# Kernel tuning notes

Measured on AMD Instinct MI355X. Metric: run time of the kernel, lower is better.

## Reference

```python
import jax, jax.numpy as jnp
import numpy as np

EMBED_DIM = 1024
NUM_HEADS = 16
HEAD_DIM = EMBED_DIM // NUM_HEADS
FEATURE_EPS = 1e-06
DEN_EPS = 1e-06


def setup_inputs() -> dict:
    key = jax.random.key(0)
    k_x, k_qw, k_qb, k_ow, k_ob = jax.random.split(key, 5)
    b, l = 2, 2048
    x = jax.random.normal(k_x, (b, l, EMBED_DIM), dtype=jnp.float32)
    s = 1.0 / np.sqrt(EMBED_DIM)
    qkv_w = jax.random.uniform(k_qw, (3 * EMBED_DIM, EMBED_DIM), minval=-s, maxval=s, dtype=jnp.float32)
    qkv_b = jax.random.uniform(k_qb, (3 * EMBED_DIM,), minval=-s, maxval=s, dtype=jnp.float32)
    out_w = jax.random.uniform(k_ow, (EMBED_DIM, EMBED_DIM), minval=-s, maxval=s, dtype=jnp.float32)
    out_b = jax.random.uniform(k_ob, (EMBED_DIM,), minval=-s, maxval=s, dtype=jnp.float32)
    return {"x": x, "qkv_w": qkv_w, "qkv_b": qkv_b, "out_w": out_w, "out_b": out_b}


def reference(x, qkv_w, qkv_b, out_w, out_b):
    b, l, e = x.shape
    # qkv projection -> (3, b, h, l, d)
    qkv = (x @ qkv_w.T + qkv_b).reshape(b, l, 3, NUM_HEADS, HEAD_DIM)
    qkv = jnp.transpose(qkv, (2, 0, 3, 1, 4))
    q, k, v = qkv[0], qkv[1], qkv[2]
    # phi(x) = relu(x) + eps
    q = jax.nn.relu(q) + FEATURE_EPS
    k = jax.nn.relu(k) + FEATURE_EPS
    # running outer-product state: (b, h, l, d, d)
    kv = jnp.cumsum(jnp.einsum('bhld,bhle->bhlde', k, v), axis=2)
    k_cum = jnp.cumsum(k, axis=2)
    num = jnp.einsum('bhld,bhlde->bhle', q, kv)
    den = jnp.maximum(jnp.einsum('bhld,bhld->bhl', q, k_cum)[..., None], DEN_EPS)
    out = num / den  # (b, h, l, d)
    out = jnp.transpose(out, (0, 2, 1, 3)).reshape(b, l, e)
    return out @ out_w.T + out_b
```

## Files before the change

### kernel.cpp

```cpp
#include <hip/hip_runtime.h>
#include <hip/hip_bf16.h>
#include <cstdint>

#define B_ 2
#define L_ 2048
#define E_ 1024
#define H_ 16
#define D_ 64
#define N3_ 3072
#define NCHUNK 32
#define CHUNK 64

typedef __attribute__((ext_vector_type(8))) short bf16x8;
typedef __attribute__((ext_vector_type(4))) float f32x4;

__device__ __forceinline__ unsigned short f2bf(float f) {
  unsigned u = __float_as_uint(f);
  unsigned r = (u + 0x7fffu + ((u >> 16) & 1u)) >> 16;
  return (unsigned short)r;
}
__device__ __forceinline__ float bf2f(unsigned short u) {
  return __uint_as_float(((unsigned)u) << 16);
}

__global__ __launch_bounds__(256) void k_cvt_all(
    const float* __restrict__ x, const float* __restrict__ qkv_w,
    const float* __restrict__ out_w, unsigned short* __restrict__ xb,
    unsigned short* __restrict__ wqkv, unsigned short* __restrict__ wout) {
  const int i = blockIdx.x * 256 + threadIdx.x;
  const float* src;
  unsigned short* dst;
  int j;
  if (i < 1048576)      { src = x;     dst = xb;   j = i; }
  else if (i < 1835008) { src = qkv_w; dst = wqkv; j = i - 1048576; }
  else                  { src = out_w; dst = wout; j = i - 1835008; }
  float4 v = reinterpret_cast<const float4*>(src)[j];
  ushort4 o;
  o.x = f2bf(v.x); o.y = f2bf(v.y); o.z = f2bf(v.z); o.w = f2bf(v.w);
  reinterpret_cast<ushort4*>(dst)[j] = o;
}

__global__ __launch_bounds__(512, 2) void k_gemm256_qkv(
    const unsigned short* __restrict__ A,
    const unsigned short* __restrict__ Bm,
    const float* __restrict__ bias,
    unsigned short* __restrict__ Qb, unsigned short* __restrict__ Kb,
    unsigned short* __restrict__ Vb) {
  __shared__ short As[2][256 * 64];
  __shared__ short Bs[2][192 * 64];
  const int tid = threadIdx.x;
  const int lane = tid & 63, wave = tid >> 6;
  const int wm = wave >> 2, wn = wave & 3;
  const int bid0 = blockIdx.y * 16 + blockIdx.x;
  const int bid = (bid0 & 7) * 32 + (bid0 >> 3);
  const int m0 = (bid >> 4) * 256, n0 = (bid & 15) * 192;
  const int srow = tid >> 3, scol = (tid & 7) * 8;
  const int ssw = (srow & 7) * 8;
  const int l15 = lane & 15, l16 = lane >> 4;
  const int sw = (l15 & 7) * 8;
  const int NT = 16;

  f32x4 acc[8][3];
#pragma unroll
  for (int i = 0; i < 8; ++i)
#pragma unroll
    for (int j = 0; j < 3; ++j) acc[i][j] = (f32x4){0.f, 0.f, 0.f, 0.f};

  auto stageA = [&](int d, int kt) {
#pragma unroll
    for (int i = 0; i < 4; ++i) {
      const int r = i * 64 + srow;
      const unsigned short* src = &A[(size_t)(m0 + r) * 1024 + kt * 64 + (scol ^ ssw)];
      __builtin_amdgcn_global_load_lds(
          (const __attribute__((address_space(1))) unsigned int*)src,
          (__attribute__((address_space(3))) unsigned int*)&As[d][r * 64 + scol], 16, 0, 0);
    }
  };
  auto stageB = [&](int d, int kt) {
#pragma unroll
    for (int i = 0; i < 3; ++i) {
      const int r = i * 64 + srow;
      const unsigned short* src = &Bm[(size_t)(n0 + r) * 1024 + kt * 64 + (scol ^ ssw)];
      __builtin_amdgcn_global_load_lds(
          (const __attribute__((address_space(1))) unsigned int*)src,
          (__attribute__((address_space(3))) unsigned int*)&Bs[d][r * 64 + scol], 16, 0, 0);
    }
  };
  auto lda = [&](bf16x8 (&dv)[8], int d, int kh) {
#pragma unroll
    for (int mi = 0; mi < 8; ++mi) {
      const int r = wm * 128 + mi * 16 + l15;
      dv[mi] = *reinterpret_cast<const bf16x8*>(&As[d][r * 64 + ((l16 * 8 + kh * 32) ^ sw)]);
    }
  };
  auto ldb = [&](bf16x8 (&dv)[3], int d, int kh) {
#pragma unroll
    for (int ni = 0; ni < 3; ++ni) {
      const int r = wn * 48 + ni * 16 + l15;
      dv[ni] = *reinterpret_cast<const bf16x8*>(&Bs[d][r * 64 + ((l16 * 8 + kh * 32) ^ sw)]);
    }
  };
  auto quad = [&](const bf16x8 (&af)[8], const bf16x8 (&bf)[3], int nb, int ne) {
    __builtin_amdgcn_s_setprio(1);
#pragma unroll
    for (int mi = 0; mi < 8; ++mi)
      for (int nn = nb; nn < ne; ++nn)
        acc[mi][nn] = __builtin_amdgcn_mfma_f32_16x16x32_bf16(af[mi], bf[nn], acc[mi][nn], 0, 0, 0);
    __builtin_amdgcn_s_setprio(0);
  };

  stageA(0, 0); stageB(0, 0); stageA(1, 1);
  asm volatile("s_waitcnt vmcnt(4)" ::: "memory");
  __builtin_amdgcn_s_barrier();

  bf16x8 af0[8], af1[8], bf0[3], bf1[3];
  for (int t = 0; t < NT; ++t) {
    const int d = t & 1;
    lda(af0, d, 0); ldb(bf0, d, 0);
    if (t + 1 < NT) stageB(d ^ 1, t + 1);
    __builtin_amdgcn_s_barrier();
    asm volatile("s_waitcnt lgkmcnt(0)" ::: "memory");
    __builtin_amdgcn_sched_barrier(0);
    quad(af0, bf0, 0, 2);
    __builtin_amdgcn_s_barrier();
    lda(af1, d, 1); ldb(bf1, d, 1);
    __builtin_amdgcn_s_barrier();
    asm volatile("s_waitcnt lgkmcnt(0)" ::: "memory");
    __builtin_amdgcn_sched_barrier(0);
    quad(af0, bf0, 2, 3);
    __builtin_amdgcn_s_barrier();
    if (t + 2 < NT) stageA(d, t + 2);
    quad(af1, bf1, 0, 2);
    __builtin_amdgcn_s_barrier();
    quad(af1, bf1, 2, 3);
    if (t + 2 < NT) asm volatile("s_waitcnt vmcnt(4)" ::: "memory");
    else            asm volatile("s_waitcnt vmcnt(0)" ::: "memory");
    __builtin_amdgcn_s_barrier();
  }

#pragma unroll
  for (int mi = 0; mi < 8; ++mi) {
#pragma unroll
    for (int ni = 0; ni < 3; ++ni) {
      const int col = n0 + wn * 48 + ni * 16 + l15;
      const float bv = bias[col];
      const int t = col >> 10, hd = col & 1023;
      const int h = hd >> 6, dd = hd & 63;
#pragma unroll
      for (int j = 0; j < 4; ++j) {
        const int row = m0 + wm * 128 + mi * 16 + l16 * 4 + j;
        const float val = acc[mi][ni][j] + bv;
        const int b = row >> 11, l = row & 2047;
        const size_t dst = (((size_t)(b * 16 + h)) * 2048 + l) * 64 + dd;
        if (t == 0)      Qb[dst] = f2bf(fmaxf(val, 0.f) + 1e-6f);
        else if (t == 1) Kb[dst] = f2bf(fmaxf(val, 0.f) + 1e-6f);
        else             Vb[dst] = f2bf(val);
      }
    }
  }
}

__global__ __launch_bounds__(512, 2) void k_gemm256_out(
    const unsigned short* __restrict__ A,
    const unsigned short* __restrict__ Bm,
    const float* __restrict__ bias, float* __restrict__ O) {
  __shared__ short As[2][256 * 64];
  __shared__ short Bs[2][64 * 64];
  const int tid = threadIdx.x;
  const int lane = tid & 63, wave = tid >> 6;
  const int wm = wave >> 2, wn = wave & 3;
  const int bid0 = blockIdx.y * 16 + blockIdx.x;
  const int bid = (bid0 & 7) * 32 + (bid0 >> 3);
  const int m0 = (bid >> 4) * 256, n0 = (bid & 15) * 64;
  const int srow = tid >> 3, scol = (tid & 7) * 8;
  const int ssw = (srow & 7) * 8;
  const int l15 = lane & 15, l16 = lane >> 4;
  const int sw = (l15 & 7) * 8;
  const int NT = 16;

  f32x4 acc[8];
#pragma unroll
  for (int i = 0; i < 8; ++i) acc[i] = (f32x4){0.f, 0.f, 0.f, 0.f};

  auto stageA = [&](int d, int kt) {
#pragma unroll
    for (int i = 0; i < 4; ++i) {
      const int r = i * 64 + srow;
      const unsigned short* src = &A[(size_t)(m0 + r) * 1024 + kt * 64 + (scol ^ ssw)];
      __builtin_amdgcn_global_load_lds(
          (const __attribute__((address_space(1))) unsigned int*)src,
          (__attribute__((address_space(3))) unsigned int*)&As[d][r * 64 + scol], 16, 0, 0);
    }
  };
  auto stageB = [&](int d, int kt) {
    const unsigned short* src = &Bm[(size_t)(n0 + srow) * 1024 + kt * 64 + (scol ^ ssw)];
    __builtin_amdgcn_global_load_lds(
        (const __attribute__((address_space(1))) unsigned int*)src,
        (__attribute__((address_space(3))) unsigned int*)&Bs[d][srow * 64 + scol], 16, 0, 0);
  };
  auto lda = [&](bf16x8 (&dv)[8], int d, int kh) {
#pragma unroll
    for (int mi = 0; mi < 8; ++mi) {
      const int r = wm * 128 + mi * 16 + l15;
      dv[mi] = *reinterpret_cast<const bf16x8*>(&As[d][r * 64 + ((l16 * 8 + kh * 32) ^ sw)]);
    }
  };
  auto ldb = [&](bf16x8& dv, int d, int kh) {
    const int r = wn * 16 + l15;
    dv = *reinterpret_cast<const bf16x8*>(&Bs[d][r * 64 + ((l16 * 8 + kh * 32) ^ sw)]);
  };
  auto half = [&](const bf16x8 (&af)[8], const bf16x8& bf, int mb) {
    __builtin_amdgcn_s_setprio(1);
#pragma unroll
    for (int mi = mb; mi < mb + 4; ++mi)
      acc[mi] = __builtin_amdgcn_mfma_f32_16x16x32_bf16(af[mi], bf, acc[mi], 0, 0, 0);
    __builtin_amdgcn_s_setprio(0);
  };

  stageA(0, 0); stageB(0, 0); stageA(1, 1);
  asm volatile("s_waitcnt vmcnt(4)" ::: "memory");
  __builtin_amdgcn_s_barrier();

  bf16x8 af0[8], af1[8], bf0, bf1;
  for (int t = 0; t < NT; ++t) {
    const int d = t & 1;
    lda(af0, d, 0); ldb(bf0, d, 0);
    if (t + 1 < NT) stageB(d ^ 1, t + 1);
    __builtin_amdgcn_s_barrier();
    asm volatile("s_waitcnt lgkmcnt(0)" ::: "memory");
    __builtin_amdgcn_sched_barrier(0);
    half(af0, bf0, 0);
    __builtin_amdgcn_s_barrier();
    lda(af1, d, 1); ldb(bf1, d, 1);
    __builtin_amdgcn_s_barrier();
    asm volatile("s_waitcnt lgkmcnt(0)" ::: "memory");
    __builtin_amdgcn_sched_barrier(0);
    half(af0, bf0, 4);
    __builtin_amdgcn_s_barrier();
    if (t + 2 < NT) stageA(d, t + 2);
    half(af1, bf1, 0);
    __builtin_amdgcn_s_barrier();
    half(af1, bf1, 4);
    if (t + 2 < NT) asm volatile("s_waitcnt vmcnt(4)" ::: "memory");
    else            asm volatile("s_waitcnt vmcnt(0)" ::: "memory");
    __builtin_amdgcn_s_barrier();
  }

  const int col = n0 + wn * 16 + l15;
  const float bv = bias[col];
#pragma unroll
  for (int mi = 0; mi < 8; ++mi) {
#pragma unroll
    for (int j = 0; j < 4; ++j) {
      const int row = m0 + wm * 128 + mi * 16 + l16 * 4 + j;
      O[(size_t)row * 1024 + col] = acc[mi][j] + bv;
    }
  }
}

__global__ __launch_bounds__(128) void k_chunkB(
    const unsigned short* __restrict__ Kb, const unsigned short* __restrict__ Vb,
    unsigned short* __restrict__ STc, unsigned short* __restrict__ Vtb) {
  __shared__ __align__(16) unsigned short Kt[64 * 72];
  __shared__ __align__(16) unsigned short Vt[64 * 72];
  const int tid = threadIdx.x;
  const int lane = tid & 63, w = tid >> 6;
  const int c = lane & 15, g = lane >> 4;
  const int bid = blockIdx.x;
  const int bh = bid >> 5, ch = bid & 31;
  const size_t base = ((size_t)bh * L_ + (size_t)ch * CHUNK) * D_;
  const int l = tid >> 1, hf = tid & 1;
  bf16x8 kv[4], vv[4];
#pragma unroll
  for (int i = 0; i < 4; ++i) {
    kv[i] = *reinterpret_cast<const bf16x8*>(&Kb[base + (size_t)l * 64 + hf * 32 + i * 8]);
    vv[i] = *reinterpret_cast<const bf16x8*>(&Vb[base + (size_t)l * 64 + hf * 32 + i * 8]);
  }
#pragma unroll
  for (int i = 0; i < 4; ++i)
#pragma unroll
    for (int r = 0; r < 8; ++r) {
      const int d = hf * 32 + i * 8 + r;
      Kt[d * 72 + l] = (unsigned short)kv[i][r];
      Vt[d * 72 + l] = (unsigned short)vv[i][r];
    }
  __syncthreads();
  bf16x8 kf[4][2], vf[2][2];
#pragma unroll
  for (int dt = 0; dt < 4; ++dt)
#pragma unroll
    for (int kh = 0; kh < 2; ++kh)
      kf[dt][kh] = *reinterpret_cast<const bf16x8*>(&Kt[(dt * 16 + c) * 72 + g * 8 + kh * 32]);
#pragma unroll
  for (int ei = 0; ei < 2; ++ei)
#pragma unroll
    for (int kh = 0; kh < 2; ++kh)
      vf[ei][kh] = *reinterpret_cast<const bf16x8*>(&Vt[((w * 2 + ei) * 16 + c) * 72 + g * 8 + kh * 32]);
  f32x4 acc[2][4];
#pragma unroll
  for (int ei = 0; ei < 2; ++ei)
#pragma unroll
    for (int dt = 0; dt < 4; ++dt) acc[ei][dt] = (f32x4){0.f, 0.f, 0.f, 0.f};
#pragma unroll
  for (int ei = 0; ei < 2; ++ei)
#pragma unroll
    for (int dt = 0; dt < 4; ++dt)
#pragma unroll
      for (int kh = 0; kh < 2; ++kh)
        acc[ei][dt] = __builtin_amdgcn_mfma_f32_16x16x32_bf16(vf[ei][kh], kf[dt][kh], acc[ei][dt], 0, 0, 0);
  const size_t stbase = (size_t)bid * 5120;
#pragma unroll
  for (int ei = 0; ei < 2; ++ei)
#pragma unroll
    for (int dt = 0; dt < 4; ++dt)
#pragma unroll
      for (int r = 0; r < 4; ++r)
        STc[stbase + (size_t)((w * 2 + ei) * 16 + 4 * g + r) * 64 + dt * 16 + c] = f2bf(acc[ei][dt][r]);
#pragma unroll
  for (int ei = 0; ei < 2; ++ei)
#pragma unroll
    for (int kh = 0; kh < 2; ++kh)
      *reinterpret_cast<bf16x8*>(&Vtb[(size_t)bid * 4096 + ((w * 2 + ei) * 16 + c) * 64 + g * 8 + kh * 32]) = vf[ei][kh];
  if (w == 0) {
    const short one = (c == 0) ? (short)0x3F80 : (short)0;
    bf16x8 of;
#pragma unroll
    for (int r = 0; r < 8; ++r) of[r] = one;
    f32x4 az[4];
#pragma unroll
    for (int dt = 0; dt < 4; ++dt) az[dt] = (f32x4){0.f, 0.f, 0.f, 0.f};
#pragma unroll
    for (int dt = 0; dt < 4; ++dt)
#pragma unroll
      for (int kh = 0; kh < 2; ++kh)
        az[dt] = __builtin_amdgcn_mfma_f32_16x16x32_bf16(of, kf[dt][kh], az[dt], 0, 0, 0);
    if (g == 0) {
#pragma unroll
      for (int dt = 0; dt < 4; ++dt)
        STc[stbase + 64 * 64 + dt * 16 + c] = f2bf(az[dt][0]);
    }
  }
}

__global__ __launch_bounds__(256) void k_prefix2(const unsigned short* __restrict__ STc,
                                                 unsigned short* __restrict__ STb) {
  const int bh = blockIdx.x;
  const int e = blockIdx.y * 256 + threadIdx.x;
  if (e >= 4160) return;
  const size_t base = (size_t)bh * NCHUNK * 5120 + e;
  float run = 0.f;
  for (int cc = 0; cc < NCHUNK; ++cc) {
    const float t = bf2f(STc[base + (size_t)cc * 5120]);
    STb[base + (size_t)cc * 5120] = f2bf(run);
    run += t;
  }
}

__global__ __launch_bounds__(256) void k_chunkD(
    const unsigned short* __restrict__ Qb, const unsigned short* __restrict__ Kb,
    const unsigned short* __restrict__ Vtb, const unsigned short* __restrict__ STb,
    unsigned short* __restrict__ attnb) {
  __shared__ __align__(16) unsigned short P[4][1024];
  const int tid = threadIdx.x;
  const int lane = tid & 63, lt = tid >> 6;
  const int c = lane & 15, g = lane >> 4;
  const int bid = blockIdx.x;
  const int bh = bid >> 5, ch = bid & 31;
  const int b = bh >> 4, h = bh & 15;
  const size_t qkbase = ((size_t)bh * L_ + (size_t)ch * CHUNK) * D_;
  bf16x8 q[2], k4[4][2], s[5][2], vt[4][2], pa[2];
#pragma unroll
  for (int kh = 0; kh < 2; ++kh)
    q[kh] = *reinterpret_cast<const bf16x8*>(&Qb[qkbase + (size_t)(lt * 16 + c) * 64 + g * 8 + kh * 32]);
#pragma unroll
  for (int jt = 0; jt < 4; ++jt)
#pragma unroll
    for (int kh = 0; kh < 2; ++kh)
      k4[jt][kh] = *reinterpret_cast<const bf16x8*>(&Kb[qkbase + (size_t)(jt * 16 + c) * 64 + g * 8 + kh * 32]);
  const size_t stbase = (size_t)bid * 5120;
#pragma unroll
  for (int et = 0; et < 5; ++et)
#pragma unroll
    for (int kh = 0; kh < 2; ++kh)
      s[et][kh] = *reinterpret_cast<const bf16x8*>(&STb[stbase + (size_t)(et * 16 + c) * 64 + g * 8 + kh * 32]);
#pragma unroll
  for (int et = 0; et < 4; ++et)
#pragma unroll
    for (int kh = 0; kh < 2; ++kh)
      vt[et][kh] = *reinterpret_cast<const bf16x8*>(&Vtb[(size_t)bid * 4096 + (size_t)(et * 16 + c) * 64 + g * 8 + kh * 32]);

  char* Pb = (char*)&P[lt][0];
  const int swz = (c & 7) << 4;
#pragma unroll
  for (int jt = 0; jt < 4; ++jt) {
    unsigned pk0 = 0, pk1 = 0;
    if (jt <= lt) {
      f32x4 a1 = (f32x4){0.f, 0.f, 0.f, 0.f};
#pragma unroll
      for (int kh = 0; kh < 2; ++kh)
        a1 = __builtin_amdgcn_mfma_f32_16x16x32_bf16(k4[jt][kh], q[kh], a1, 0, 0, 0);
      if (jt == lt) {
#pragma unroll
        for (int r = 0; r < 4; ++r) a1[r] = (4 * g + r <= c) ? a1[r] : 0.f;
      }
      pk0 = (unsigned)f2bf(a1[0]) | ((unsigned)f2bf(a1[1]) << 16);
      pk1 = (unsigned)f2bf(a1[2]) | ((unsigned)f2bf(a1[3]) << 16);
    }
    *reinterpret_cast<unsigned*>(Pb + ((c * 128 + 32 * jt + 8 * g + 0) ^ swz)) = pk0;
    *reinterpret_cast<unsigned*>(Pb + ((c * 128 + 32 * jt + 8 * g + 4) ^ swz)) = pk1;
  }
#pragma unroll
  for (int kh = 0; kh < 2; ++kh)
    pa[kh] = *reinterpret_cast<const bf16x8*>(Pb + (c * 128 + ((16 * g + 64 * kh) ^ swz)));

  f32x4 acc2[5];
#pragma unroll
  for (int et = 0; et < 5; ++et) acc2[et] = (f32x4){0.f, 0.f, 0.f, 0.f};
  const short one = (c == 0) ? (short)0x3F80 : (short)0;
  bf16x8 of;
#pragma unroll
  for (int r = 0; r < 8; ++r) of[r] = one;
#pragma unroll
  for (int et = 0; et < 5; ++et) {
#pragma unroll
    for (int kh = 0; kh < 2; ++kh) {
      acc2[et] = __builtin_amdgcn_mfma_f32_16x16x32_bf16(q[kh], s[et][kh], acc2[et], 0, 0, 0);
      bf16x8 vv = (et < 4) ? vt[et][kh] : of;
      acc2[et] = __builtin_amdgcn_mfma_f32_16x16x32_bf16(pa[kh], vv, acc2[et], 0, 0, 0);
    }
  }
  float inv[4];
#pragma unroll
  for (int r = 0; r < 4; ++r) {
    float dv = __shfl(acc2[4][r], lane & 48, 64);
    inv[r] = 1.f / fmaxf(dv, 1e-6f);
  }
  const size_t obase = ((size_t)b * L_ + (size_t)ch * CHUNK + (size_t)lt * 16) * E_ + (size_t)h * 64;
#pragma unroll
  for (int et = 0; et < 4; ++et)
#pragma unroll
    for (int r = 0; r < 4; ++r)
      attnb[obase + (size_t)(4 * g + r) * E_ + et * 16 + c] = f2bf(acc2[et][r] * inv[r]);
}

extern "C" void kernel_launch(void* const* d_in, const int* in_sizes, int n_in,
                              void* d_out, int out_size, void* d_ws, size_t ws_size,
                              hipStream_t stream) {
  const float* x = (const float*)d_in[0];
  const float* qkv_w = (const float*)d_in[1];
  const float* qkv_b = (const float*)d_in[2];
  const float* out_w = (const float*)d_in[3];
  const float* out_b = (const float*)d_in[4];
  float* out = (float*)d_out;

  const size_t SZ = (size_t)B_ * H_ * L_ * D_;
  char* p = (char*)d_ws;
  unsigned short* Qb = (unsigned short*)p;    p += SZ * 2;
  unsigned short* Kb = (unsigned short*)p;    p += SZ * 2;
  unsigned short* Vb = (unsigned short*)p;    p += SZ * 2;
  unsigned short* Vtb = (unsigned short*)p;   p += (size_t)1024 * 4096 * 2;
  unsigned short* STc = (unsigned short*)p;   p += (size_t)1024 * 5120 * 2;
  unsigned short* STb = (unsigned short*)p;   p += (size_t)1024 * 5120 * 2;
  unsigned short* xb = (unsigned short*)p;    p += SZ * 2;
  unsigned short* wqkv = (unsigned short*)p;  p += (size_t)N3_ * E_ * 2;
  unsigned short* wout = (unsigned short*)p;  p += (size_t)E_ * E_ * 2;
  unsigned short* attnb = (unsigned short*)p; p += SZ * 2;

  dim3 blk(256);
  k_cvt_all<<<dim3(8192), blk, 0, stream>>>(x, qkv_w, out_w, xb, wqkv, wout);
  k_gemm256_qkv<<<dim3(16, 16), dim3(512), 0, stream>>>(xb, wqkv, qkv_b, Qb, Kb, Vb);
  k_chunkB<<<dim3(1024), dim3(128), 0, stream>>>(Kb, Vb, STc, Vtb);
  k_prefix2<<<dim3(32, 17), blk, 0, stream>>>(STc, STb);
  k_chunkD<<<dim3(1024), blk, 0, stream>>>(Qb, Kb, Vtb, STb, attnb);
  k_gemm256_out<<<dim3(16, 16), dim3(512), 0, stream>>>(attnb, wout, out_b, out);
}
```

Before: 163.6 us.

## Write transposed K and V tiles from QKV GEMM epilogue, drop chunkB transpose

The QKV GEMM epilogue now writes K and V directly in a per-chunk transposed layout (d-major within each 64-token chunk), alongside the row-major K still needed by chunkD. chunkB then loads its MFMA fragments straight from global memory instead of staging a shared-memory transpose, and it no longer writes Vtb. This removes a global read of K/V, the LDS transpose, a barrier and a Vtb write in chunkB. In exchange the GEMM epilogue performs an extra scattered 2-byte store for K, and its transposed stores have poor coalescing.

```diff
diff --git a/kernel.cpp b/kernel.cpp
--- a/kernel.cpp
+++ b/kernel.cpp
@@ -45,7 +45,7 @@
     const unsigned short* __restrict__ Bm,
     const float* __restrict__ bias,
     unsigned short* __restrict__ Qb, unsigned short* __restrict__ Kb,
-    unsigned short* __restrict__ Vb) {
+    unsigned short* __restrict__ Ktb, unsigned short* __restrict__ Vtb) {
   __shared__ short As[2][256 * 64];
   __shared__ short Bs[2][192 * 64];
   const int tid = threadIdx.x;
@@ -151,10 +151,18 @@
         const int row = m0 + wm * 128 + mi * 16 + l16 * 4 + j;
         const float val = acc[mi][ni][j] + bv;
         const int b = row >> 11, l = row & 2047;
-        const size_t dst = (((size_t)(b * 16 + h)) * 2048 + l) * 64 + dd;
-        if (t == 0)      Qb[dst] = f2bf(fmaxf(val, 0.f) + 1e-6f);
-        else if (t == 1) Kb[dst] = f2bf(fmaxf(val, 0.f) + 1e-6f);
-        else             Vb[dst] = f2bf(val);
+        const int bh = b * 16 + h;
+        const size_t dst = ((size_t)bh * 2048 + l) * 64 + dd;
+        const size_t tdst = ((size_t)(bh * 32 + (l >> 6))) * 4096 + (size_t)dd * 64 + (l & 63);
+        if (t == 0) {
+          Qb[dst] = f2bf(fmaxf(val, 0.f) + 1e-6f);
+        } else if (t == 1) {
+          const unsigned short kv2 = f2bf(fmaxf(val, 0.f) + 1e-6f);
+          Kb[dst] = kv2;
+          Ktb[tdst] = kv2;
+        } else {
+          Vtb[tdst] = f2bf(val);
+        }
       }
     }
   }
@@ -259,43 +267,24 @@
 }
 
 __global__ __launch_bounds__(128) void k_chunkB(
-    const unsigned short* __restrict__ Kb, const unsigned short* __restrict__ Vb,
-    unsigned short* __restrict__ STc, unsigned short* __restrict__ Vtb) {
-  __shared__ __align__(16) unsigned short Kt[64 * 72];
-  __shared__ __align__(16) unsigned short Vt[64 * 72];
+    const unsigned short* __restrict__ Ktb, const unsigned short* __restrict__ Vtb,
+    unsigned short* __restrict__ STc) {
   const int tid = threadIdx.x;
   const int lane = tid & 63, w = tid >> 6;
   const int c = lane & 15, g = lane >> 4;
   const int bid = blockIdx.x;
-  const int bh = bid >> 5, ch = bid & 31;
-  const size_t base = ((size_t)bh * L_ + (size_t)ch * CHUNK) * D_;
-  const int l = tid >> 1, hf = tid & 1;
-  bf16x8 kv[4], vv[4];
-#pragma unroll
-  for (int i = 0; i < 4; ++i) {
-    kv[i] = *reinterpret_cast<const bf16x8*>(&Kb[base + (size_t)l * 64 + hf * 32 + i * 8]);
-    vv[i] = *reinterpret_cast<const bf16x8*>(&Vb[base + (size_t)l * 64 + hf * 32 + i * 8]);
-  }
-#pragma unroll
-  for (int i = 0; i < 4; ++i)
-#pragma unroll
-    for (int r = 0; r < 8; ++r) {
-      const int d = hf * 32 + i * 8 + r;
-      Kt[d * 72 + l] = (unsigned short)kv[i][r];
-      Vt[d * 72 + l] = (unsigned short)vv[i][r];
-    }
-  __syncthreads();
+  const size_t tb = (size_t)bid * 4096;
   bf16x8 kf[4][2], vf[2][2];
 #pragma unroll
   for (int dt = 0; dt < 4; ++dt)
 #pragma unroll
     for (int kh = 0; kh < 2; ++kh)
-      kf[dt][kh] = *reinterpret_cast<const bf16x8*>(&Kt[(dt * 16 + c) * 72 + g * 8 + kh * 32]);
+      kf[dt][kh] = *reinterpret_cast<const bf16x8*>(&Ktb[tb + (size_t)(dt * 16 + c) * 64 + g * 8 + kh * 32]);
 #pragma unroll
   for (int ei = 0; ei < 2; ++ei)
 #pragma unroll
     for (int kh = 0; kh < 2; ++kh)
-      vf[ei][kh] = *reinterpret_cast<const bf16x8*>(&Vt[((w * 2 + ei) * 16 + c) * 72 + g * 8 + kh * 32]);
+      vf[ei][kh] = *reinterpret_cast<const bf16x8*>(&Vtb[tb + (size_t)((w * 2 + ei) * 16 + c) * 64 + g * 8 + kh * 32]);
   f32x4 acc[2][4];
 #pragma unroll
   for (int ei = 0; ei < 2; ++ei)
@@ -316,11 +305,6 @@
 #pragma unroll
       for (int r = 0; r < 4; ++r)
         STc[stbase + (size_t)((w * 2 + ei) * 16 + 4 * g + r) * 64 + dt * 16 + c] = f2bf(acc[ei][dt][r]);
-#pragma unroll
-  for (int ei = 0; ei < 2; ++ei)
-#pragma unroll
-    for (int kh = 0; kh < 2; ++kh)
-      *reinterpret_cast<bf16x8*>(&Vtb[(size_t)bid * 4096 + ((w * 2 + ei) * 16 + c) * 64 + g * 8 + kh * 32]) = vf[ei][kh];
   if (w == 0) {
     const short one = (c == 0) ? (short)0x3F80 : (short)0;
     bf16x8 of;
@@ -457,7 +441,7 @@
   char* p = (char*)d_ws;
   unsigned short* Qb = (unsigned short*)p;    p += SZ * 2;
   unsigned short* Kb = (unsigned short*)p;    p += SZ * 2;
-  unsigned short* Vb = (unsigned short*)p;    p += SZ * 2;
+  unsigned short* Ktb = (unsigned short*)p;   p += (size_t)1024 * 4096 * 2;
   unsigned short* Vtb = (unsigned short*)p;   p += (size_t)1024 * 4096 * 2;
   unsigned short* STc = (unsigned short*)p;   p += (size_t)1024 * 5120 * 2;
   unsigned short* STb = (unsigned short*)p;   p += (size_t)1024 * 5120 * 2;
@@ -468,8 +452,8 @@
 
   dim3 blk(256);
   k_cvt_all<<<dim3(8192), blk, 0, stream>>>(x, qkv_w, out_w, xb, wqkv, wout);
-  k_gemm256_qkv<<<dim3(16, 16), dim3(512), 0, stream>>>(xb, wqkv, qkv_b, Qb, Kb, Vb);
-  k_chunkB<<<dim3(1024), dim3(128), 0, stream>>>(Kb, Vb, STc, Vtb);
+  k_gemm256_qkv<<<dim3(16, 16), dim3(512), 0, stream>>>(xb, wqkv, qkv_b, Qb, Kb, Ktb, Vtb);
+  k_chunkB<<<dim3(1024), dim3(128), 0, stream>>>(Ktb, Vtb, STc);
   k_prefix2<<<dim3(32, 17), blk, 0, stream>>>(STc, STb);
   k_chunkD<<<dim3(1024), blk, 0, stream>>>(Qb, Kb, Vtb, STb, attnb);
   k_gemm256_out<<<dim3(16, 16), dim3(512), 0, stream>>>(attnb, wout, out_b, out);
```

Measured after the change: 178.9 us. +9.4%, slower.
